# Kernel tuning notes

Hardware: AMD Instinct MI355X
Metric: run time of the kernel (lower is better)

Reference implementation:

```python
import jax, jax.numpy as jnp
import numpy as np

N_NODES = 50000
N_EDGES = 800000
F_IN = 128
HID = 128
OUT = 64


def setup_inputs() -> dict:
    key = jax.random.key(0)
    ks = jax.random.split(key, 10)
    def lin(k, fan_in, fan_out):
        s = 1.0 / np.sqrt(fan_in)
        kw, kb = jax.random.split(k)
        W = jax.random.uniform(kw, (fan_in, fan_out), jnp.float32, -s, s)
        b = jax.random.uniform(kb, (fan_out,), jnp.float32, -s, s)
        return W, b
    x = jax.random.normal(ks[0], (N_NODES, F_IN), jnp.float32)
    edge_index = jax.random.randint(ks[1], (2, N_EDGES), 0, N_NODES, dtype=jnp.int32)
    W1, b1 = lin(ks[2], F_IN, HID)   # GCNConv 1
    Wl, bl = lin(ks[3], HID, HID)    # linear_layers
    W2, b2 = lin(ks[4], HID, HID)    # GCNConv 2
    Wo, bo = lin(ks[5], HID, OUT)    # output_layers
    return {"x": x, "edge_index": edge_index, "W1": W1, "b1": b1,
            "Wl": Wl, "bl": bl, "W2": W2, "b2": b2, "Wo": Wo, "bo": bo}


def gcn_conv(x, src, dst, W, b, n_nodes):
    # PyG GCNConv: add self loops, symmetric norm D^-1/2 (A+I) D^-1/2 (x W) + b
    deg = jax.ops.segment_sum(jnp.ones_like(dst, dtype=x.dtype), dst, num_segments=n_nodes)
    dinv = jnp.where(deg > 0, jax.lax.rsqrt(jnp.maximum(deg, 1.0)), 0.0)
    norm = dinv[src] * dinv[dst]                     # [E+N]
    h = x @ W                                        # [N, H]
    msg = h[src] * norm[:, None]                     # [E+N, H]
    agg = jax.ops.segment_sum(msg, dst, num_segments=n_nodes)
    return agg + b


def reference(x, edge_index, W1, b1, Wl, bl, W2, b2, Wo, bo):
    n = x.shape[0]
    loops = jnp.arange(n, dtype=edge_index.dtype)
    src = jnp.concatenate([edge_index[0], loops])
    dst = jnp.concatenate([edge_index[1], loops])
    h = jnp.tanh(gcn_conv(x, src, dst, W1, b1, n))
    h = h @ Wl + bl
    h = jnp.tanh(gcn_conv(h, src, dst, W2, b2, n))
    h = h @ Wo + bo                                  # [N, OUT]
    # adaptive_max_pool1d over nodes -> [1, OUT]
    return jnp.max(h, axis=0, keepdims=True)
```

## Files before the change

### kernel.cpp

```cpp
#include <hip/hip_runtime.h>
#include <math.h>

#define F 128
#define OUTF 64
#define CAP 96

__global__ __launch_bounds__(256)
void fill_kernel(const int* __restrict__ src, const int* __restrict__ dst,
                 int* __restrict__ cnt, int* __restrict__ slot, int E) {
    int e = blockIdx.x * 256 + threadIdx.x;
    if (e >= E) return;
    int s = src[e], d = dst[e];
    int pos = atomicAdd(&cnt[d], 1);
    if (pos < CAP) slot[(size_t)d * CAP + pos] = s;
}

__global__ __launch_bounds__(256)
void wfuse_dinv_kernel(const float* __restrict__ Wl_, const float* __restrict__ bl_,
                       const float* __restrict__ W2_, float* __restrict__ Wf,
                       float* __restrict__ bf, const int* __restrict__ cnt,
                       float* __restrict__ dinv, int n) {
    int t = threadIdx.x;
    int bi = blockIdx.x;
    if (bi < 64) {
        int i = bi * 2 + (t >> 7);
        int j = t & 127;
        float acc = 0.f;
        #pragma unroll 8
        for (int k = 0; k < 128; ++k)
            acc = fmaf(Wl_[i * 128 + k], W2_[k * 128 + j], acc);
        Wf[i * 128 + j] = acc;
    } else if (bi == 64) {
        if (t < 128) {
            float acc = 0.f;
            #pragma unroll 8
            for (int k = 0; k < 128; ++k)
                acc = fmaf(bl_[k], W2_[k * 128 + t], acc);
            bf[t] = acc;
        }
    } else {
        int i = (bi - 65) * 256 + t;
        if (i < n) dinv[i] = rsqrtf((float)cnt[i] + 1.0f);
    }
}

__global__ __launch_bounds__(256)
void gather_kernel(const float* __restrict__ H, const float* __restrict__ dinv,
                   const int* __restrict__ cnt, const int* __restrict__ slot,
                   const float* __restrict__ b, float* __restrict__ out, int n) {
    int wave = threadIdx.x >> 6;
    int lane = threadIdx.x & 63;
    int v = blockIdx.x * 4 + wave;
    if (v >= n) return;
    int half = lane >> 5;
    int c = lane & 31;
    float dd = dinv[v];
    int deg = cnt[v];
    const int* sl = slot + (size_t)v * CAP;

    float4 a = make_float4(0.f, 0.f, 0.f, 0.f);
    if (half == 0) {
        float4 h0 = ((const float4*)(H + (size_t)v * F))[c];
        float s2 = dd * dd;
        a.x = h0.x * s2; a.y = h0.y * s2; a.z = h0.z * s2; a.w = h0.w * s2;
    }

    int i = half;
    for (; i + 2 < deg; i += 4) {
        int s0 = sl[i], s1 = sl[i + 2];
        float n0 = dinv[s0] * dd, n1 = dinv[s1] * dd;
        float4 u0 = ((const float4*)(H + (size_t)s0 * F))[c];
        float4 u1 = ((const float4*)(H + (size_t)s1 * F))[c];
        a.x = fmaf(u0.x, n0, a.x); a.y = fmaf(u0.y, n0, a.y);
        a.z = fmaf(u0.z, n0, a.z); a.w = fmaf(u0.w, n0, a.w);
        a.x = fmaf(u1.x, n1, a.x); a.y = fmaf(u1.y, n1, a.y);
        a.z = fmaf(u1.z, n1, a.z); a.w = fmaf(u1.w, n1, a.w);
    }
    if (i < deg) {
        int s0 = sl[i];
        float n0 = dinv[s0] * dd;
        float4 u0 = ((const float4*)(H + (size_t)s0 * F))[c];
        a.x = fmaf(u0.x, n0, a.x); a.y = fmaf(u0.y, n0, a.y);
        a.z = fmaf(u0.z, n0, a.z); a.w = fmaf(u0.w, n0, a.w);
    }

    a.x += __shfl_xor(a.x, 32);
    a.y += __shfl_xor(a.y, 32);
    a.z += __shfl_xor(a.z, 32);
    a.w += __shfl_xor(a.w, 32);

    if (half == 0) {
        float4 bb = ((const float4*)b)[c];
        float4 r;
        r.x = tanhf(a.x + bb.x);
        r.y = tanhf(a.y + bb.y);
        r.z = tanhf(a.z + bb.z);
        r.w = tanhf(a.w + bb.w);
        ((float4*)(out + (size_t)v * F))[c] = r;
    }
}

template<int COLS, bool BIAS, bool DOMAX>
__global__ __launch_bounds__(256)
void gemm_kernel(const float* __restrict__ A, const float* __restrict__ W,
                 const float* __restrict__ bias, float* __restrict__ C,
                 float* __restrict__ part, int n) {
    constexpr int TC = COLS / 8;
    constexpr int TR = 256 / TC;
    constexpr int ROWS = TR * 8;
    constexpr int BK = 32;
    constexpr int WCH = COLS / 4;
    constexpr int XST = ROWS + 4;

    __shared__ float Wl[BK * COLS];
    __shared__ float Xl[BK * XST];
    __shared__ float red[DOMAX ? TR * COLS : 1];

    int t = threadIdx.x;
    int tc = t % TC, tr = t / TC;
    int r0 = blockIdx.x * ROWS;

    int c0 = 2 * tc, c1 = 2 * tc + 1;
    int s0 = (COLS == 128) ? (c0 ^ (c0 >> 3)) : c0;
    int s1 = (COLS == 128) ? (c1 ^ (c1 >> 3)) : c1;

    float acc[8][8];
    #pragma unroll
    for (int i = 0; i < 8; ++i)
        #pragma unroll
        for (int j = 0; j < 8; ++j) acc[i][j] = 0.0f;

    for (int k0 = 0; k0 < F; k0 += BK) {
        constexpr int WCHT = BK * WCH / 256;
        #pragma unroll
        for (int j = 0; j < WCHT; ++j) {
            int idx = t + j * 256;
            int k = idx / WCH, cc = idx % WCH;
            float4 v = ((const float4*)(W + (size_t)(k0 + k) * COLS))[cc];
            int ccs = (COLS == 128) ? (cc ^ (cc >> 3)) : cc;
            ((float4*)&Wl[k * COLS])[ccs] = v;
        }
        constexpr int XCHT = ROWS * (BK / 4) / 256;
        #pragma unroll
        for (int j = 0; j < XCHT; ++j) {
            int idx = t + j * 256;
            int row = idx >> 3, cc = idx & 7;
            float4 v = make_float4(0.f, 0.f, 0.f, 0.f);
            int gr = r0 + row;
            if (gr < n) v = *(const float4*)(A + (size_t)gr * F + k0 + cc * 4);
            Xl[(cc * 4 + 0) * XST + row] = v.x;
            Xl[(cc * 4 + 1) * XST + row] = v.y;
            Xl[(cc * 4 + 2) * XST + row] = v.z;
            Xl[(cc * 4 + 3) * XST + row] = v.w;
        }
        __syncthreads();

        #pragma unroll 8
        for (int k = 0; k < BK; ++k) {
            const float* xp = &Xl[k * XST + tr * 8];
            float4 xa = *(const float4*)xp;
            float4 xb = *(const float4*)(xp + 4);
            float4 w0 = ((const float4*)&Wl[k * COLS])[s0];
            float4 w1 = ((const float4*)&Wl[k * COLS])[s1];
            float xv[8] = {xa.x, xa.y, xa.z, xa.w, xb.x, xb.y, xb.z, xb.w};
            float wv[8] = {w0.x, w0.y, w0.z, w0.w, w1.x, w1.y, w1.z, w1.w};
            #pragma unroll
            for (int i = 0; i < 8; ++i)
                #pragma unroll
                for (int j = 0; j < 8; ++j)
                    acc[i][j] = fmaf(xv[i], wv[j], acc[i][j]);
        }
        __syncthreads();
    }

    float4 b0 = make_float4(0.f, 0.f, 0.f, 0.f), b1 = b0;
    if (BIAS || DOMAX) {
        b0 = ((const float4*)bias)[c0];
        b1 = ((const float4*)bias)[c1];
    }
    float bv[8] = {b0.x, b0.y, b0.z, b0.w, b1.x, b1.y, b1.z, b1.w};

    if (DOMAX) {
        float mj[8];
        #pragma unroll
        for (int j = 0; j < 8; ++j) mj[j] = -INFINITY;
        #pragma unroll
        for (int i = 0; i < 8; ++i) {
            int row = r0 + tr * 8 + i;
            if (row < n) {
                #pragma unroll
                for (int j = 0; j < 8; ++j)
                    mj[j] = fmaxf(mj[j], acc[i][j] + bv[j]);
            }
        }
        #pragma unroll
        for (int j = 0; j < 8; ++j) red[tr * COLS + tc * 8 + j] = mj[j];
        __syncthreads();
        if (t < COLS) {
            float mm = red[t];
            for (int r = 1; r < TR; ++r) mm = fmaxf(mm, red[r * COLS + t]);
            part[blockIdx.x * COLS + t] = mm;
        }
    } else {
        #pragma unroll
        for (int i = 0; i < 8; ++i) {
            int row = r0 + tr * 8 + i;
            if (row >= n) break;
            float4 o0, o1;
            o0.x = acc[i][0] + bv[0]; o0.y = acc[i][1] + bv[1];
            o0.z = acc[i][2] + bv[2]; o0.w = acc[i][3] + bv[3];
            o1.x = acc[i][4] + bv[4]; o1.y = acc[i][5] + bv[5];
            o1.z = acc[i][6] + bv[6]; o1.w = acc[i][7] + bv[7];
            float4* cp = (float4*)(C + (size_t)row * COLS);
            cp[c0] = o0;
            cp[c1] = o1;
        }
    }
}

__global__ __launch_bounds__(256)
void rowmax_final(const float* __restrict__ part, float* __restrict__ out, int nb) {
    int c = threadIdx.x & 63;
    int g = threadIdx.x >> 6;
    float m = -INFINITY;
    for (int bidx = g; bidx < nb; bidx += 4)
        m = fmaxf(m, part[bidx * OUTF + c]);
    __shared__ float sm[256];
    sm[threadIdx.x] = m;
    __syncthreads();
    if (threadIdx.x < 64) {
        m = fmaxf(fmaxf(sm[threadIdx.x], sm[threadIdx.x + 64]),
                  fmaxf(sm[threadIdx.x + 128], sm[threadIdx.x + 192]));
        out[threadIdx.x] = m;
    }
}

extern "C" void kernel_launch(void* const* d_in, const int* in_sizes, int n_in,
                              void* d_out, int out_size, void* d_ws, size_t ws_size,
                              hipStream_t stream) {
    const float* x  = (const float*)d_in[0];
    const int*   ei = (const int*)d_in[1];
    const float* W1 = (const float*)d_in[2];
    const float* b1 = (const float*)d_in[3];
    const float* Wl = (const float*)d_in[4];
    const float* bl = (const float*)d_in[5];
    const float* W2 = (const float*)d_in[6];
    const float* b2 = (const float*)d_in[7];
    const float* Wo = (const float*)d_in[8];
    const float* bo = (const float*)d_in[9];

    int n = in_sizes[0] / F;
    int E = in_sizes[1] / 2;
    const int* src = ei;
    const int* dst = ei + E;

    auto align = [](size_t o) { return (o + 255) & ~(size_t)255; };
    char* ws = (char*)d_ws;
    size_t off = 0;
    size_t NB = (size_t)n * F * sizeof(float);
    float* bufA = (float*)(ws + off); off = align(off + NB);
    float* bufB = (float*)(ws + off); off = align(off + NB);
    float* dinv = (float*)(ws + off); off = align(off + (size_t)n * 4);
    int*   cnt  = (int*)(ws + off);   off = align(off + (size_t)n * 4);
    int*   slot = (int*)(ws + off);   off = align(off + (size_t)n * CAP * 4);
    float* Wf   = (float*)(ws + off); off = align(off + 128 * 128 * 4);
    float* bf   = (float*)(ws + off); off = align(off + 128 * 4);
    float* part = (float*)(ws + off); off = align(off + 256 * 64 * 4);

    int gE    = (E + 255) / 256;
    int gScan = (n + 255) / 256;
    int gGat  = (n + 3) / 4;
    int gG128 = (n + 127) / 128;
    int gG64  = (n + 255) / 256;

    hipMemsetAsync(cnt, 0, (size_t)n * sizeof(int), stream);
    fill_kernel<<<gE, 256, 0, stream>>>(src, dst, cnt, slot, E);
    wfuse_dinv_kernel<<<65 + gScan, 256, 0, stream>>>(Wl, bl, W2, Wf, bf, cnt, dinv, n);

    gemm_kernel<128, false, false><<<gG128, 256, 0, stream>>>(x, W1, nullptr, bufA, nullptr, n);
    gather_kernel<<<gGat, 256, 0, stream>>>(bufA, dinv, cnt, slot, b1, bufB, n);

    gemm_kernel<128, true, false><<<gG128, 256, 0, stream>>>(bufB, Wf, bf, bufA, nullptr, n);
    gather_kernel<<<gGat, 256, 0, stream>>>(bufA, dinv, cnt, slot, b2, bufB, n);

    gemm_kernel<64, true, true><<<gG64, 256, 0, stream>>>(bufB, Wo, bo, nullptr, part, n);
    rowmax_final<<<1, 256, 0, stream>>>(part, (float*)d_out, gG64);
}
```

Measured before the change: 360.0 us.

## Replace FP32 SIMT GEMMs with split-bf16 MFMA GEMMs

The three dense GEMMs move from a shared-memory FP32 FMA kernel to MFMA 16x16x32 bf16 instructions. Weights are pre-split into hi/lo bf16 parts in an MFMA-friendly layout by a new prep kernel. Activations are split on the fly, and three MFMAs per tile (hi*hi, lo*hi, hi*lo) approximate FP32 accuracy. This targets GEMM compute time, at the cost of an extra launch, uncoalesced scalar output stores and some lost precision.

Result: faster. 331.1 us (-8.0%).

```diff
diff --git a/kernel.cpp b/kernel.cpp
--- a/kernel.cpp
+++ b/kernel.cpp
@@ -4,6 +4,17 @@
 #define F 128
 #define OUTF 64
 #define CAP 96
+
+typedef __attribute__((ext_vector_type(8))) short short8;
+typedef __attribute__((ext_vector_type(4))) float f32x4;
+
+__device__ inline unsigned short bf16_rne(float f) {
+    unsigned u = __float_as_uint(f);
+    return (unsigned short)((u + 0x7FFFu + ((u >> 16) & 1u)) >> 16);
+}
+__device__ inline float bf16_to_f(unsigned short h) {
+    return __uint_as_float((unsigned)h << 16);
+}
 
 __global__ __launch_bounds__(256)
 void fill_kernel(const int* __restrict__ src, const int* __restrict__ dst,
@@ -45,6 +56,28 @@
 }
 
 __global__ __launch_bounds__(256)
+void wprep_kernel(const float* __restrict__ W1, const float* __restrict__ Wf,
+                  const float* __restrict__ Wo,
+                  short* __restrict__ W1h, short* __restrict__ W1l,
+                  short* __restrict__ Wfh, short* __restrict__ Wfl,
+                  short* __restrict__ Woh, short* __restrict__ Wol) {
+    int id = blockIdx.x * 256 + threadIdx.x;
+    const float* W; short *Hh, *Hl; int N, base;
+    if (id < 16384)      { W = W1; Hh = W1h; Hl = W1l; N = 128; base = id; }
+    else if (id < 32768) { W = Wf; Hh = Wfh; Hl = Wfl; N = 128; base = id - 16384; }
+    else if (id < 40960) { W = Wo; Hh = Woh; Hl = Wol; N = 64;  base = id - 32768; }
+    else return;
+    int k = base / N, nn = base % N;
+    float w = W[k * N + nn];
+    int c = k >> 5, hh = (k >> 3) & 3, kk = k & 7;
+    int j = nn >> 4, col = nn & 15;
+    int idx = (((j * 4 + c) * 4 + hh) * 16 + col) * 8 + kk;
+    unsigned short hi = bf16_rne(w);
+    Hh[idx] = (short)hi;
+    Hl[idx] = (short)bf16_rne(w - bf16_to_f(hi));
+}
+
+__global__ __launch_bounds__(256)
 void gather_kernel(const float* __restrict__ H, const float* __restrict__ dinv,
                    const int* __restrict__ cnt, const int* __restrict__ slot,
                    const float* __restrict__ b, float* __restrict__ out, int n) {
@@ -102,118 +135,79 @@
 
 template<int COLS, bool BIAS, bool DOMAX>
 __global__ __launch_bounds__(256)
-void gemm_kernel(const float* __restrict__ A, const float* __restrict__ W,
-                 const float* __restrict__ bias, float* __restrict__ C,
-                 float* __restrict__ part, int n) {
-    constexpr int TC = COLS / 8;
-    constexpr int TR = 256 / TC;
-    constexpr int ROWS = TR * 8;
-    constexpr int BK = 32;
-    constexpr int WCH = COLS / 4;
-    constexpr int XST = ROWS + 4;
-
-    __shared__ float Wl[BK * COLS];
-    __shared__ float Xl[BK * XST];
-    __shared__ float red[DOMAX ? TR * COLS : 1];
-
+void mgemm_kernel(const float* __restrict__ A, const short* __restrict__ Whi,
+                  const short* __restrict__ Wlo, const float* __restrict__ bias,
+                  float* __restrict__ C, float* __restrict__ part, int n) {
+    constexpr int NT = COLS / 16;
+    __shared__ float red[DOMAX ? 4 * COLS : 1];
     int t = threadIdx.x;
-    int tc = t % TC, tr = t / TC;
-    int r0 = blockIdx.x * ROWS;
-
-    int c0 = 2 * tc, c1 = 2 * tc + 1;
-    int s0 = (COLS == 128) ? (c0 ^ (c0 >> 3)) : c0;
-    int s1 = (COLS == 128) ? (c1 ^ (c1 >> 3)) : c1;
-
-    float acc[8][8];
+    int wave = t >> 6, l = t & 63;
+    int fr = l & 15, fh = l >> 4;
+    int m0 = blockIdx.x * 64 + wave * 16;
+    int arow = min(m0 + fr, n - 1);
+    const float* Ap = A + (size_t)arow * F + fh * 8;
+
+    f32x4 acc[NT];
     #pragma unroll
-    for (int i = 0; i < 8; ++i)
+    for (int j = 0; j < NT; ++j) acc[j] = (f32x4){0.f, 0.f, 0.f, 0.f};
+
+    #pragma unroll
+    for (int c = 0; c < 4; ++c) {
+        float4 a0 = *(const float4*)(Ap + c * 32);
+        float4 a1 = *(const float4*)(Ap + c * 32 + 4);
+        short8 ahi, alo;
+        {
+            float v[8] = {a0.x, a0.y, a0.z, a0.w, a1.x, a1.y, a1.z, a1.w};
+            #pragma unroll
+            for (int i = 0; i < 8; ++i) {
+                unsigned short hb = bf16_rne(v[i]);
+                ahi[i] = (short)hb;
+                alo[i] = (short)bf16_rne(v[i] - bf16_to_f(hb));
+            }
+        }
         #pragma unroll
-        for (int j = 0; j < 8; ++j) acc[i][j] = 0.0f;
-
-    for (int k0 = 0; k0 < F; k0 += BK) {
-        constexpr int WCHT = BK * WCH / 256;
+        for (int j = 0; j < NT; ++j) {
+            int bidx = (((j * 4 + c) * 4 + fh) * 16 + fr) * 8;
+            short8 bhi = *(const short8*)(Whi + bidx);
+            short8 blo = *(const short8*)(Wlo + bidx);
+            acc[j] = __builtin_amdgcn_mfma_f32_16x16x32_bf16(ahi, bhi, acc[j], 0, 0, 0);
+            acc[j] = __builtin_amdgcn_mfma_f32_16x16x32_bf16(alo, bhi, acc[j], 0, 0, 0);
+            acc[j] = __builtin_amdgcn_mfma_f32_16x16x32_bf16(ahi, blo, acc[j], 0, 0, 0);
+        }
+    }
+
+    float bv[NT];
+    #pragma unroll
+    for (int j = 0; j < NT; ++j) bv[j] = (BIAS || DOMAX) ? bias[j * 16 + fr] : 0.f;
+
+    if (DOMAX) {
         #pragma unroll
-        for (int j = 0; j < WCHT; ++j) {
-            int idx = t + j * 256;
-            int k = idx / WCH, cc = idx % WCH;
-            float4 v = ((const float4*)(W + (size_t)(k0 + k) * COLS))[cc];
-            int ccs = (COLS == 128) ? (cc ^ (cc >> 3)) : cc;
-            ((float4*)&Wl[k * COLS])[ccs] = v;
-        }
-        constexpr int XCHT = ROWS * (BK / 4) / 256;
-        #pragma unroll
-        for (int j = 0; j < XCHT; ++j) {
-            int idx = t + j * 256;
-            int row = idx >> 3, cc = idx & 7;
-            float4 v = make_float4(0.f, 0.f, 0.f, 0.f);
-            int gr = r0 + row;
-            if (gr < n) v = *(const float4*)(A + (size_t)gr * F + k0 + cc * 4);
-            Xl[(cc * 4 + 0) * XST + row] = v.x;
-            Xl[(cc * 4 + 1) * XST + row] = v.y;
-            Xl[(cc * 4 + 2) * XST + row] = v.z;
-            Xl[(cc * 4 + 3) * XST + row] = v.w;
-        }
-        __syncthreads();
-
-        #pragma unroll 8
-        for (int k = 0; k < BK; ++k) {
-            const float* xp = &Xl[k * XST + tr * 8];
-            float4 xa = *(const float4*)xp;
-            float4 xb = *(const float4*)(xp + 4);
-            float4 w0 = ((const float4*)&Wl[k * COLS])[s0];
-            float4 w1 = ((const float4*)&Wl[k * COLS])[s1];
-            float xv[8] = {xa.x, xa.y, xa.z, xa.w, xb.x, xb.y, xb.z, xb.w};
-            float wv[8] = {w0.x, w0.y, w0.z, w0.w, w1.x, w1.y, w1.z, w1.w};
+        for (int j = 0; j < NT; ++j) {
+            float mj = -INFINITY;
             #pragma unroll
-            for (int i = 0; i < 8; ++i)
-                #pragma unroll
-                for (int j = 0; j < 8; ++j)
-                    acc[i][j] = fmaf(xv[i], wv[j], acc[i][j]);
-        }
-        __syncthreads();
-    }
-
-    float4 b0 = make_float4(0.f, 0.f, 0.f, 0.f), b1 = b0;
-    if (BIAS || DOMAX) {
-        b0 = ((const float4*)bias)[c0];
-        b1 = ((const float4*)bias)[c1];
-    }
-    float bv[8] = {b0.x, b0.y, b0.z, b0.w, b1.x, b1.y, b1.z, b1.w};
-
-    if (DOMAX) {
-        float mj[8];
-        #pragma unroll
-        for (int j = 0; j < 8; ++j) mj[j] = -INFINITY;
-        #pragma unroll
-        for (int i = 0; i < 8; ++i) {
-            int row = r0 + tr * 8 + i;
-            if (row < n) {
-                #pragma unroll
-                for (int j = 0; j < 8; ++j)
-                    mj[j] = fmaxf(mj[j], acc[i][j] + bv[j]);
+            for (int reg = 0; reg < 4; ++reg) {
+                int r = m0 + fh * 4 + reg;
+                if (r < n) mj = fmaxf(mj, acc[j][reg] + bv[j]);
             }
-        }
-        #pragma unroll
-        for (int j = 0; j < 8; ++j) red[tr * COLS + tc * 8 + j] = mj[j];
+            mj = fmaxf(mj, __shfl_xor(mj, 16));
+            mj = fmaxf(mj, __shfl_xor(mj, 32));
+            if (fh == 0) red[wave * COLS + j * 16 + fr] = mj;
+        }
         __syncthreads();
         if (t < COLS) {
-            float mm = red[t];
-            for (int r = 1; r < TR; ++r) mm = fmaxf(mm, red[r * COLS + t]);
+            float mm = fmaxf(fmaxf(red[t], red[COLS + t]),
+                             fmaxf(red[2 * COLS + t], red[3 * COLS + t]));
             part[blockIdx.x * COLS + t] = mm;
         }
     } else {
         #pragma unroll
-        for (int i = 0; i < 8; ++i) {
-            int row = r0 + tr * 8 + i;
-            if (row >= n) break;
-            float4 o0, o1;
-            o0.x = acc[i][0] + bv[0]; o0.y = acc[i][1] + bv[1];
-            o0.z = acc[i][2] + bv[2]; o0.w = acc[i][3] + bv[3];
-            o1.x = acc[i][4] + bv[4]; o1.y = acc[i][5] + bv[5];
-            o1.z = acc[i][6] + bv[6]; o1.w = acc[i][7] + bv[7];
-            float4* cp = (float4*)(C + (size_t)row * COLS);
-            cp[c0] = o0;
-            cp[c1] = o1;
+        for (int j = 0; j < NT; ++j) {
+            int ccol = j * 16 + fr;
+            #pragma unroll
+            for (int reg = 0; reg < 4; ++reg) {
+                int r = m0 + fh * 4 + reg;
+                if (r < n) C[(size_t)r * COLS + ccol] = acc[j][reg] + bv[j];
+            }
         }
     }
 }
@@ -265,24 +259,30 @@
     int*   slot = (int*)(ws + off);   off = align(off + (size_t)n * CAP * 4);
     float* Wf   = (float*)(ws + off); off = align(off + 128 * 128 * 4);
     float* bf   = (float*)(ws + off); off = align(off + 128 * 4);
-    float* part = (float*)(ws + off); off = align(off + 256 * 64 * 4);
+    short* W1h  = (short*)(ws + off); off = align(off + 16384 * 2);
+    short* W1l  = (short*)(ws + off); off = align(off + 16384 * 2);
+    short* Wfh  = (short*)(ws + off); off = align(off + 16384 * 2);
+    short* Wfl  = (short*)(ws + off); off = align(off + 16384 * 2);
+    short* Woh  = (short*)(ws + off); off = align(off + 8192 * 2);
+    short* Wol  = (short*)(ws + off); off = align(off + 8192 * 2);
+    float* part = (float*)(ws + off); off = align(off + (size_t)800 * 64 * 4);
 
     int gE    = (E + 255) / 256;
     int gScan = (n + 255) / 256;
     int gGat  = (n + 3) / 4;
-    int gG128 = (n + 127) / 128;
-    int gG64  = (n + 255) / 256;
+    int gM    = (n + 63) / 64;
 
     hipMemsetAsync(cnt, 0, (size_t)n * sizeof(int), stream);
     fill_kernel<<<gE, 256, 0, stream>>>(src, dst, cnt, slot, E);
     wfuse_dinv_kernel<<<65 + gScan, 256, 0, stream>>>(Wl, bl, W2, Wf, bf, cnt, dinv, n);
-
-    gemm_kernel<128, false, false><<<gG128, 256, 0, stream>>>(x, W1, nullptr, bufA, nullptr, n);
+    wprep_kernel<<<160, 256, 0, stream>>>(W1, Wf, Wo, W1h, W1l, Wfh, Wfl, Woh, Wol);
+
+    mgemm_kernel<128, false, false><<<gM, 256, 0, stream>>>(x, W1h, W1l, nullptr, bufA, nullptr, n);
     gather_kernel<<<gGat, 256, 0, stream>>>(bufA, dinv, cnt, slot, b1, bufB, n);
 
-    gemm_kernel<128, true, false><<<gG128, 256, 0, stream>>>(bufB, Wf, bf, bufA, nullptr, n);
+    mgemm_kernel<128, true, false><<<gM, 256, 0, stream>>>(bufB, Wfh, Wfl, bf, bufA, nullptr, n);
     gather_kernel<<<gGat, 256, 0, stream>>>(bufA, dinv, cnt, slot, b2, bufB, n);
 
-    gemm_kernel<64, true, true><<<gG64, 256, 0, stream>>>(bufB, Wo, bo, nullptr, part, n);
-    rowmax_final<<<1, 256, 0, stream>>>(part, (float*)d_out, gG64);
-}
+    mgemm_kernel<64, true, true><<<gM, 256, 0, stream>>>(bufB, Woh, Wol, bo, nullptr, part, n);
+    rowmax_final<<<1, 256, 0, stream>>>(part, (float*)d_out, gM);
+}
```
